# Performance work log

Measured on AMD Instinct MI355X. Metric: run time of the kernel, lower is better.

Reference implementation:

```python
import jax, jax.numpy as jnp
import numpy as np

D_MODEL = 1024
NUM_HEADS = 16
HEAD_DIM = D_MODEL // NUM_HEADS


def setup_inputs() -> dict:
    key = jax.random.key(0)
    ks = jax.random.split(key, 5)
    B, S = 2, 2048
    x = jax.random.normal(ks[0], (B, S, D_MODEL), dtype=jnp.float32)
    # nn.Linear(d,d,bias=False): y = x @ W.T, W is [out,in]. Init ~ U(-1/sqrt(d), 1/sqrt(d)).
    lim = 1.0 / np.sqrt(D_MODEL)
    wq = jax.random.uniform(ks[1], (D_MODEL, D_MODEL), jnp.float32, -lim, lim)
    wk = jax.random.uniform(ks[2], (D_MODEL, D_MODEL), jnp.float32, -lim, lim)
    wv = jax.random.uniform(ks[3], (D_MODEL, D_MODEL), jnp.float32, -lim, lim)
    wo = jax.random.uniform(ks[4], (D_MODEL, D_MODEL), jnp.float32, -lim, lim)
    return {"x": x, "wq": wq, "wk": wk, "wv": wv, "wo": wo}


def reference(x, wq, wk, wv, wo):
    B, S, D = x.shape
    H, Hd = NUM_HEADS, HEAD_DIM
    scale = Hd ** 0.5
    # projections (torch Linear: x @ W.T), split heads -> [B,H,S,Hd]
    q = (x @ wq.T).reshape(B, S, H, Hd).transpose(0, 2, 1, 3)
    k = (x @ wk.T).reshape(B, S, H, Hd).transpose(0, 2, 1, 3)
    v = (x @ wv.T).reshape(B, S, H, Hd).transpose(0, 2, 1, 3)
    scores = jnp.einsum('bhqd,bhkd->bhqk', q, k) / scale  # [B,H,S,S]
    # causal mask: disallow j > i
    causal_mask = jnp.triu(jnp.ones((S, S), dtype=bool), k=1)
    scores = jnp.where(causal_mask, -jnp.inf, scores)
    attn = jax.nn.softmax(scores, axis=-1)
    out = jnp.einsum('bhqk,bhkd->bhqd', attn, v)
    out = out.transpose(0, 2, 1, 3).reshape(B, S, D)
    return out @ wo.T
```

## Files before the change

kernel.cpp:

```cpp
#include <hip/hip_runtime.h>

#define DEV __device__ __forceinline__

typedef __attribute__((ext_vector_type(4))) float f32x4;
typedef __attribute__((ext_vector_type(8))) __bf16 bf16x8;

typedef __attribute__((address_space(1))) const uint32_t gu32;
typedef __attribute__((address_space(3))) uint32_t su32;

DEV void gload16(const void* g, void* s) {
  __builtin_amdgcn_global_load_lds((gu32*)(uintptr_t)g,
                                   (su32*)(uint32_t)(uintptr_t)s, 16, 0, 0);
}

DEV ushort f2bf(float f) {
  unsigned u = __builtin_bit_cast(unsigned, f);
  u = (u + 0x7fffu + ((u >> 16) & 1u)) >> 16;
  return (ushort)u;
}

DEV bf16x8 lds8(const ushort* p) {
  return __builtin_bit_cast(bf16x8, *(const uint4*)(p));
}

__global__ void cvt_bf16(const float* __restrict__ src, ushort* __restrict__ dst, int n4) {
  int i = blockIdx.x * blockDim.x + threadIdx.x;
  if (i >= n4) return;
  float4 v = ((const float4*)src)[i];
  ushort4 o;
  o.x = f2bf(v.x); o.y = f2bf(v.y); o.z = f2bf(v.z); o.w = f2bf(v.w);
  ((ushort4*)dst)[i] = o;
}

template <int F32OUT>
DEV void gemm_core(const ushort* __restrict__ A, const ushort* __restrict__ W,
                   void* __restrict__ Cout, ushort* sA, ushort* sB) {
  const int tid = threadIdx.x;
  const int l = tid & 63, wv = tid >> 6;
  const int g = l >> 4, lan = l & 15;
  const int wr = wv >> 1, wc = wv & 1;
  const int brow = blockIdx.y * 128, bcol = blockIdx.x * 128;

  f32x4 acc[4][4] = {};

  for (int k0 = 0; k0 < 1024; k0 += 32) {
    __syncthreads();
#pragma unroll
    for (int i = 0; i < 2; ++i) {
      int n = i * 256 + wv * 64 + l;
      int row = n >> 2;
      int ss = n & 3;
      int gs = (ss - (row >> 1)) & 3;
      gload16(A + (size_t)(brow + row) * 1024 + k0 + gs * 8,
              sA + (size_t)(i * 256 + wv * 64) * 8);
      gload16(W + (size_t)(bcol + row) * 1024 + k0 + gs * 8,
              sB + (size_t)(i * 256 + wv * 64) * 8);
    }
    __syncthreads();

    bf16x8 a[4], b[4];
#pragma unroll
    for (int fr = 0; fr < 4; ++fr) {
      int row = wr * 64 + fr * 16 + lan;
      a[fr] = lds8(sA + row * 32 + 8 * (((row >> 1) + g) & 3));
    }
#pragma unroll
    for (int fn = 0; fn < 4; ++fn) {
      int row = wc * 64 + fn * 16 + lan;
      b[fn] = lds8(sB + row * 32 + 8 * (((row >> 1) + g) & 3));
    }
#pragma unroll
    for (int fr = 0; fr < 4; ++fr)
#pragma unroll
      for (int fn = 0; fn < 4; ++fn)
        acc[fr][fn] = __builtin_amdgcn_mfma_f32_16x16x32_bf16(a[fr], b[fn], acc[fr][fn], 0, 0, 0);
  }

#pragma unroll
  for (int fr = 0; fr < 4; ++fr)
#pragma unroll
    for (int fn = 0; fn < 4; ++fn)
#pragma unroll
      for (int r = 0; r < 4; ++r) {
        int row = brow + wr * 64 + fr * 16 + g * 4 + r;
        int col = bcol + wc * 64 + fn * 16 + lan;
        if (F32OUT)
          ((float*)Cout)[(size_t)row * 1024 + col] = acc[fr][fn][r];
        else
          ((ushort*)Cout)[(size_t)row * 1024 + col] = f2bf(acc[fr][fn][r]);
      }
}

__global__ __launch_bounds__(256) void gemm_qkv(
    const ushort* __restrict__ X, const ushort* __restrict__ Wq,
    const ushort* __restrict__ Wk, const ushort* __restrict__ Wv,
    ushort* __restrict__ Q, ushort* __restrict__ K, ushort* __restrict__ V) {
  __shared__ __align__(16) ushort sA[4096];
  __shared__ __align__(16) ushort sB[4096];
  const ushort* W = blockIdx.z == 0 ? Wq : (blockIdx.z == 1 ? Wk : Wv);
  ushort* C = blockIdx.z == 0 ? Q : (blockIdx.z == 1 ? K : V);
  gemm_core<0>(X, W, (void*)C, sA, sB);
}

__global__ __launch_bounds__(256) void gemm_out(
    const ushort* __restrict__ AO, const ushort* __restrict__ Wo, float* __restrict__ C) {
  __shared__ __align__(16) ushort sA[4096];
  __shared__ __align__(16) ushort sB[4096];
  gemm_core<1>(AO, Wo, (void*)C, sA, sB);
}

__global__ __launch_bounds__(256) void vt_kernel(const ushort* __restrict__ V,
                                                 ushort* __restrict__ Vt) {
  __shared__ __align__(16) ushort T[64 * 64];
  const int tid = threadIdx.x;
  const int stile = blockIdx.x, bh = blockIdx.y;
  const int b = bh >> 4, h = bh & 15;

#pragma unroll
  for (int i = 0; i < 2; ++i) {
    int m = i * 256 + tid;
    int s = m >> 3, dc = m & 7;
    uint4 v = *(const uint4*)(V + (size_t)(b * 2048 + stile * 64 + s) * 1024 + h * 64 + dc * 8);
    *(uint4*)(T + s * 64 + ((8 * dc) ^ (((s >> 3) & 7) << 3))) = v;
  }
  __syncthreads();

#pragma unroll
  for (int i = 0; i < 2; ++i) {
    int m = i * 256 + tid;
    int d = m >> 3, sb = m & 7;
    ushort tmp[8];
#pragma unroll
    for (int e = 0; e < 8; ++e)
      tmp[e] = T[(sb * 8 + e) * 64 + (d ^ (sb << 3))];
    uint4 o;
    o.x = (uint)tmp[0] | ((uint)tmp[1] << 16);
    o.y = (uint)tmp[2] | ((uint)tmp[3] << 16);
    o.z = (uint)tmp[4] | ((uint)tmp[5] << 16);
    o.w = (uint)tmp[6] | ((uint)tmp[7] << 16);
    *(uint4*)(Vt + ((size_t)bh * 64 + d) * 2048 + stile * 64 + sb * 8) = o;
  }
}

__global__ __launch_bounds__(256) void attn_fwd(
    const ushort* __restrict__ Qm, const ushort* __restrict__ Km,
    const ushort* __restrict__ Vt, ushort* __restrict__ AO) {
  __shared__ __align__(16) ushort sK[64 * 64];
  __shared__ __align__(16) ushort sV[64 * 64];
  __shared__ __align__(16) ushort sP[4 * 16 * 64];

  const int tid = threadIdx.x;
  const int l = tid & 63, wv = tid >> 6;
  const int g = l >> 4, lan = l & 15;
  const int bid = blockIdx.x;
  const int rank = bid >> 5, bh = bid & 31;
  const int qt = 31 - rank;
  const int b = bh >> 4, h = bh & 15;
  const int q0 = qt * 64 + wv * 16;
  const int qg = q0 + lan;

  bf16x8 qf[2];
#pragma unroll
  for (int kf = 0; kf < 2; ++kf)
    qf[kf] = __builtin_bit_cast(bf16x8,
        *(const uint4*)(Qm + (size_t)(b * 2048 + qg) * 1024 + h * 64 + kf * 32 + g * 8));

  float mrun = -1e30f, lrun = 0.f;
  f32x4 o[4];
#pragma unroll
  for (int of = 0; of < 4; ++of) o[of] = (f32x4){0.f, 0.f, 0.f, 0.f};

  ushort* Pw = sP + wv * 1024;
  const int nkt = qt + 1;

  for (int kt = 0; kt < nkt; ++kt) {
    __syncthreads();
#pragma unroll
    for (int i = 0; i < 2; ++i) {
      int n = i * 256 + wv * 64 + l;
      int row = n >> 3, ss = n & 7, gs = ss ^ (row & 7);
      gload16(Km + (size_t)(b * 2048 + kt * 64 + row) * 1024 + h * 64 + gs * 8,
              sK + (size_t)(i * 256 + wv * 64) * 8);
      gload16(Vt + ((size_t)bh * 64 + row) * 2048 + kt * 64 + gs * 8,
              sV + (size_t)(i * 256 + wv * 64) * 8);
    }
    __syncthreads();

    f32x4 sc[4];
    __builtin_amdgcn_s_setprio(1);
#pragma unroll
    for (int kvf = 0; kvf < 4; ++kvf) {
      f32x4 acc = (f32x4){0.f, 0.f, 0.f, 0.f};
#pragma unroll
      for (int kf = 0; kf < 2; ++kf) {
        int row = kvf * 16 + lan;
        bf16x8 kb = lds8(sK + row * 64 + 8 * ((kf * 4 + g) ^ (row & 7)));
        acc = __builtin_amdgcn_mfma_f32_16x16x32_bf16(kb, qf[kf], acc, 0, 0, 0);
      }
      sc[kvf] = acc;
    }
    __builtin_amdgcn_s_setprio(0);

    float mx = -1e30f;
#pragma unroll
    for (int kvf = 0; kvf < 4; ++kvf)
#pragma unroll
      for (int r = 0; r < 4; ++r) {
        int kvg = kt * 64 + kvf * 16 + 4 * g + r;
        float v = sc[kvf][r] * 0.125f;
        v = (kvg <= qg) ? v : -1e30f;
        sc[kvf][r] = v;
        mx = fmaxf(mx, v);
      }
    mx = fmaxf(mx, __shfl_xor(mx, 16));
    mx = fmaxf(mx, __shfl_xor(mx, 32));
    float mnew = fmaxf(mrun, mx);
    float alpha = __expf(mrun - mnew);
    mrun = mnew;
    float rs = 0.f;
#pragma unroll
    for (int kvf = 0; kvf < 4; ++kvf)
#pragma unroll
      for (int r = 0; r < 4; ++r) {
        float p = __expf(sc[kvf][r] - mnew);
        sc[kvf][r] = p;
        rs += p;
      }
    rs += __shfl_xor(rs, 16);
    rs += __shfl_xor(rs, 32);
    lrun = lrun * alpha + rs;

#pragma unroll
    for (int kvf = 0; kvf < 4; ++kvf) {
      ushort4 pk;
      pk.x = f2bf(sc[kvf][0]); pk.y = f2bf(sc[kvf][1]);
      pk.z = f2bf(sc[kvf][2]); pk.w = f2bf(sc[kvf][3]);
      *(ushort4*)(Pw + lan * 64 + ((16 * kvf + 4 * g) ^ ((lan & 7) << 3))) = pk;
    }

    float al[4];
#pragma unroll
    for (int r = 0; r < 4; ++r) al[r] = __shfl(alpha, g * 4 + r);
#pragma unroll
    for (int of = 0; of < 4; ++of)
#pragma unroll
      for (int r = 0; r < 4; ++r) o[of][r] *= al[r];

    bf16x8 pa[2];
#pragma unroll
    for (int kf = 0; kf < 2; ++kf)
      pa[kf] = lds8(Pw + lan * 64 + ((32 * kf + 8 * g) ^ ((lan & 7) << 3)));

    __builtin_amdgcn_s_setprio(1);
#pragma unroll
    for (int of = 0; of < 4; ++of) {
#pragma unroll
      for (int kf = 0; kf < 2; ++kf) {
        int row = of * 16 + lan;
        bf16x8 vb = lds8(sV + row * 64 + 8 * ((kf * 4 + g) ^ (row & 7)));
        o[of] = __builtin_amdgcn_mfma_f32_16x16x32_bf16(pa[kf], vb, o[of], 0, 0, 0);
      }
    }
    __builtin_amdgcn_s_setprio(0);
  }

#pragma unroll
  for (int r = 0; r < 4; ++r) {
    float il = 1.0f / __shfl(lrun, g * 4 + r);
#pragma unroll
    for (int of = 0; of < 4; ++of) {
      int grow = qt * 64 + wv * 16 + g * 4 + r;
      AO[(size_t)(b * 2048 + grow) * 1024 + h * 64 + of * 16 + lan] = f2bf(o[of][r] * il);
    }
  }
}

extern "C" void kernel_launch(void* const* d_in, const int* in_sizes, int n_in,
                              void* d_out, int out_size, void* d_ws, size_t ws_size,
                              hipStream_t stream) {
  const float* x  = (const float*)d_in[0];
  const float* wq = (const float*)d_in[1];
  const float* wk = (const float*)d_in[2];
  const float* wv = (const float*)d_in[3];
  const float* wo = (const float*)d_in[4];
  float* out = (float*)d_out;

  char* ws = (char*)d_ws;
  const size_t MB = 1ull << 20;
  ushort* xb  = (ushort*)(ws + 0);
  ushort* wqb = (ushort*)(ws + 8 * MB);
  ushort* wkb = (ushort*)(ws + 10 * MB);
  ushort* wvb = (ushort*)(ws + 12 * MB);
  ushort* wob = (ushort*)(ws + 14 * MB);
  ushort* Q   = (ushort*)(ws + 16 * MB);
  ushort* K   = (ushort*)(ws + 24 * MB);
  ushort* V   = (ushort*)(ws + 32 * MB);
  ushort* AO  = (ushort*)(ws + 40 * MB);
  ushort* Vt  = (ushort*)(ws + 0);

  cvt_bf16<<<4096, 256, 0, stream>>>(x, xb, 1048576);
  cvt_bf16<<<1024, 256, 0, stream>>>(wq, wqb, 262144);
  cvt_bf16<<<1024, 256, 0, stream>>>(wk, wkb, 262144);
  cvt_bf16<<<1024, 256, 0, stream>>>(wv, wvb, 262144);
  cvt_bf16<<<1024, 256, 0, stream>>>(wo, wob, 262144);

  gemm_qkv<<<dim3(8, 32, 3), 256, 0, stream>>>(xb, wqb, wkb, wvb, Q, K, V);
  vt_kernel<<<dim3(32, 32), 256, 0, stream>>>(V, Vt);
  attn_fwd<<<1024, 256, 0, stream>>>(Q, K, Vt, AO);
  gemm_out<<<dim3(8, 32), 256, 0, stream>>>(AO, wob, out);
}
```

Baseline: 198.3 us.

## Double-buffer GEMM and attention loads, fuse conversions, fold softmax scale into Wq

Merges the five fp32-to-bf16 conversion launches into one kernel, and pre-scales Wq by log2(e)/8 so attention can use exp2 without a per-element scale. Both GEMMs and the attention loop now double-buffer their LDS tiles, so the next tile's global loads overlap the current MFMA work, with a single vmcnt wait and barrier per step. The output GEMM uses narrower 128x64 tiles to launch more blocks. Attention applies the causal mask only on the diagonal tile and skips rescaling the accumulator while the running max grows by at most 8. That skip risks a small loss of accuracy, and the extra LDS buffers can lower occupancy.

```diff
diff --git a/kernel.cpp b/kernel.cpp
--- a/kernel.cpp
+++ b/kernel.cpp
@@ -13,100 +13,132 @@
                                    (su32*)(uint32_t)(uintptr_t)s, 16, 0, 0);
 }
 
-DEV ushort f2bf(float f) {
-  unsigned u = __builtin_bit_cast(unsigned, f);
-  u = (u + 0x7fffu + ((u >> 16) & 1u)) >> 16;
-  return (ushort)u;
-}
+DEV ushort bfbits(float f) { return __builtin_bit_cast(ushort, (__bf16)f); }
 
 DEV bf16x8 lds8(const ushort* p) {
   return __builtin_bit_cast(bf16x8, *(const uint4*)(p));
 }
 
-__global__ void cvt_bf16(const float* __restrict__ src, ushort* __restrict__ dst, int n4) {
+DEV void vmcnt0bar() {
+  asm volatile("s_waitcnt vmcnt(0)" ::: "memory");
+  __builtin_amdgcn_s_barrier();
+}
+
+__global__ void cvt_all(const float* __restrict__ x, const float* __restrict__ wq,
+                        const float* __restrict__ wk, const float* __restrict__ wv,
+                        const float* __restrict__ wo, ushort* __restrict__ xb,
+                        ushort* __restrict__ wb) {
   int i = blockIdx.x * blockDim.x + threadIdx.x;
-  if (i >= n4) return;
-  float4 v = ((const float4*)src)[i];
+  const float* src; ushort* dst; float scl = 1.0f; int j;
+  if (i < 1048576) { src = x; dst = xb; j = i; }
+  else {
+    int t = (i - 1048576) >> 18;
+    j = (i - 1048576) & 262143;
+    src = t == 0 ? wq : (t == 1 ? wk : (t == 2 ? wv : wo));
+    dst = wb + t * 1048576;
+    if (t == 0) scl = 0.18033688011f;
+  }
+  float4 v = ((const float4*)src)[j];
   ushort4 o;
-  o.x = f2bf(v.x); o.y = f2bf(v.y); o.z = f2bf(v.z); o.w = f2bf(v.w);
-  ((ushort4*)dst)[i] = o;
-}
-
-template <int F32OUT>
+  o.x = bfbits(v.x * scl); o.y = bfbits(v.y * scl);
+  o.z = bfbits(v.z * scl); o.w = bfbits(v.w * scl);
+  ((ushort4*)dst)[j] = o;
+}
+
+template <int NFR, int F32OUT>
 DEV void gemm_core(const ushort* __restrict__ A, const ushort* __restrict__ W,
                    void* __restrict__ Cout, ushort* sA, ushort* sB) {
   const int tid = threadIdx.x;
   const int l = tid & 63, wv = tid >> 6;
   const int g = l >> 4, lan = l & 15;
   const int wr = wv >> 1, wc = wv & 1;
-  const int brow = blockIdx.y * 128, bcol = blockIdx.x * 128;
-
-  f32x4 acc[4][4] = {};
-
-  for (int k0 = 0; k0 < 1024; k0 += 32) {
-    __syncthreads();
+  const int brow = blockIdx.y * 128, bcol = blockIdx.x * (NFR * 32);
+  const int ASZ = 128 * 32, BSZ = NFR * 32 * 32;
+
+  f32x4 acc[4][NFR] = {};
+
+  auto stage = [&](int buf, int k0) {
+    ushort* dA = sA + buf * ASZ;
+    ushort* dB = sB + buf * BSZ;
 #pragma unroll
     for (int i = 0; i < 2; ++i) {
       int n = i * 256 + wv * 64 + l;
-      int row = n >> 2;
-      int ss = n & 3;
-      int gs = (ss - (row >> 1)) & 3;
+      int row = n >> 2, ss = n & 3, gs = (ss - (row >> 1)) & 3;
       gload16(A + (size_t)(brow + row) * 1024 + k0 + gs * 8,
-              sA + (size_t)(i * 256 + wv * 64) * 8);
+              dA + (i * 256 + wv * 64) * 8);
+    }
+#pragma unroll
+    for (int i = 0; i < NFR / 2; ++i) {
+      int n = i * 256 + wv * 64 + l;
+      int row = n >> 2, ss = n & 3, gs = (ss - (row >> 1)) & 3;
       gload16(W + (size_t)(bcol + row) * 1024 + k0 + gs * 8,
-              sB + (size_t)(i * 256 + wv * 64) * 8);
-    }
-    __syncthreads();
-
-    bf16x8 a[4], b[4];
+              dB + (i * 256 + wv * 64) * 8);
+    }
+  };
+
+  auto compute = [&](int buf) {
+    const ushort* cA = sA + buf * ASZ;
+    const ushort* cB = sB + buf * BSZ;
+    bf16x8 a[4], b[NFR];
 #pragma unroll
     for (int fr = 0; fr < 4; ++fr) {
       int row = wr * 64 + fr * 16 + lan;
-      a[fr] = lds8(sA + row * 32 + 8 * (((row >> 1) + g) & 3));
-    }
-#pragma unroll
-    for (int fn = 0; fn < 4; ++fn) {
-      int row = wc * 64 + fn * 16 + lan;
-      b[fn] = lds8(sB + row * 32 + 8 * (((row >> 1) + g) & 3));
-    }
+      a[fr] = lds8(cA + row * 32 + 8 * (((row >> 1) + g) & 3));
+    }
+#pragma unroll
+    for (int fn = 0; fn < NFR; ++fn) {
+      int row = wc * (NFR * 16) + fn * 16 + lan;
+      b[fn] = lds8(cB + row * 32 + 8 * (((row >> 1) + g) & 3));
+    }
+    __builtin_amdgcn_s_setprio(1);
 #pragma unroll
     for (int fr = 0; fr < 4; ++fr)
 #pragma unroll
-      for (int fn = 0; fn < 4; ++fn)
+      for (int fn = 0; fn < NFR; ++fn)
         acc[fr][fn] = __builtin_amdgcn_mfma_f32_16x16x32_bf16(a[fr], b[fn], acc[fr][fn], 0, 0, 0);
-  }
+    __builtin_amdgcn_s_setprio(0);
+  };
+
+  stage(0, 0);
+  vmcnt0bar();
+#pragma unroll 1
+  for (int t = 0; t < 15; ++t) {
+    stage(1, (2 * t + 1) * 32); compute(0); vmcnt0bar();
+    stage(0, (2 * t + 2) * 32); compute(1); vmcnt0bar();
+  }
+  stage(1, 31 * 32); compute(0); vmcnt0bar();
+  compute(1);
 
 #pragma unroll
   for (int fr = 0; fr < 4; ++fr)
 #pragma unroll
-    for (int fn = 0; fn < 4; ++fn)
+    for (int fn = 0; fn < NFR; ++fn)
 #pragma unroll
       for (int r = 0; r < 4; ++r) {
         int row = brow + wr * 64 + fr * 16 + g * 4 + r;
-        int col = bcol + wc * 64 + fn * 16 + lan;
+        int col = bcol + wc * (NFR * 16) + fn * 16 + lan;
         if (F32OUT)
           ((float*)Cout)[(size_t)row * 1024 + col] = acc[fr][fn][r];
         else
-          ((ushort*)Cout)[(size_t)row * 1024 + col] = f2bf(acc[fr][fn][r]);
+          ((ushort*)Cout)[(size_t)row * 1024 + col] = bfbits(acc[fr][fn][r]);
       }
 }
 
 __global__ __launch_bounds__(256) void gemm_qkv(
-    const ushort* __restrict__ X, const ushort* __restrict__ Wq,
-    const ushort* __restrict__ Wk, const ushort* __restrict__ Wv,
+    const ushort* __restrict__ X, const ushort* __restrict__ Wb,
     ushort* __restrict__ Q, ushort* __restrict__ K, ushort* __restrict__ V) {
-  __shared__ __align__(16) ushort sA[4096];
-  __shared__ __align__(16) ushort sB[4096];
-  const ushort* W = blockIdx.z == 0 ? Wq : (blockIdx.z == 1 ? Wk : Wv);
+  __shared__ __align__(16) ushort sA[2 * 128 * 32];
+  __shared__ __align__(16) ushort sB[2 * 128 * 32];
+  const ushort* W = Wb + (size_t)blockIdx.z * 1048576;
   ushort* C = blockIdx.z == 0 ? Q : (blockIdx.z == 1 ? K : V);
-  gemm_core<0>(X, W, (void*)C, sA, sB);
+  gemm_core<4, 0>(X, W, (void*)C, sA, sB);
 }
 
 __global__ __launch_bounds__(256) void gemm_out(
     const ushort* __restrict__ AO, const ushort* __restrict__ Wo, float* __restrict__ C) {
-  __shared__ __align__(16) ushort sA[4096];
-  __shared__ __align__(16) ushort sB[4096];
-  gemm_core<1>(AO, Wo, (void*)C, sA, sB);
+  __shared__ __align__(16) ushort sA[2 * 128 * 32];
+  __shared__ __align__(16) ushort sB[2 * 64 * 32];
+  gemm_core<2, 1>(AO, Wo, (void*)C, sA, sB);
 }
 
 __global__ __launch_bounds__(256) void vt_kernel(const ushort* __restrict__ V,
@@ -145,8 +177,8 @@
 __global__ __launch_bounds__(256) void attn_fwd(
     const ushort* __restrict__ Qm, const ushort* __restrict__ Km,
     const ushort* __restrict__ Vt, ushort* __restrict__ AO) {
-  __shared__ __align__(16) ushort sK[64 * 64];
-  __shared__ __align__(16) ushort sV[64 * 64];
+  __shared__ __align__(16) ushort sK[2][64 * 64];
+  __shared__ __align__(16) ushort sV[2][64 * 64];
   __shared__ __align__(16) ushort sP[4 * 16 * 64];
 
   const int tid = threadIdx.x;
@@ -173,79 +205,96 @@
   ushort* Pw = sP + wv * 1024;
   const int nkt = qt + 1;
 
-  for (int kt = 0; kt < nkt; ++kt) {
-    __syncthreads();
+  auto stagekv = [&](int buf, int kt) {
 #pragma unroll
     for (int i = 0; i < 2; ++i) {
       int n = i * 256 + wv * 64 + l;
       int row = n >> 3, ss = n & 7, gs = ss ^ (row & 7);
       gload16(Km + (size_t)(b * 2048 + kt * 64 + row) * 1024 + h * 64 + gs * 8,
-              sK + (size_t)(i * 256 + wv * 64) * 8);
+              sK[buf] + (i * 256 + wv * 64) * 8);
       gload16(Vt + ((size_t)bh * 64 + row) * 2048 + kt * 64 + gs * 8,
-              sV + (size_t)(i * 256 + wv * 64) * 8);
-    }
-    __syncthreads();
+              sV[buf] + (i * 256 + wv * 64) * 8);
+    }
+  };
+
+  stagekv(0, 0);
+  vmcnt0bar();
+
+#pragma unroll 1
+  for (int kt = 0; kt < nkt; ++kt) {
+    const int buf = kt & 1;
+    if (kt + 1 < nkt) stagekv(buf ^ 1, kt + 1);
 
     f32x4 sc[4];
     __builtin_amdgcn_s_setprio(1);
 #pragma unroll
     for (int kvf = 0; kvf < 4; ++kvf) {
-      f32x4 acc = (f32x4){0.f, 0.f, 0.f, 0.f};
+      f32x4 a2 = (f32x4){0.f, 0.f, 0.f, 0.f};
 #pragma unroll
       for (int kf = 0; kf < 2; ++kf) {
         int row = kvf * 16 + lan;
-        bf16x8 kb = lds8(sK + row * 64 + 8 * ((kf * 4 + g) ^ (row & 7)));
-        acc = __builtin_amdgcn_mfma_f32_16x16x32_bf16(kb, qf[kf], acc, 0, 0, 0);
+        bf16x8 kb = lds8(sK[buf] + row * 64 + 8 * ((kf * 4 + g) ^ (row & 7)));
+        a2 = __builtin_amdgcn_mfma_f32_16x16x32_bf16(kb, qf[kf], a2, 0, 0, 0);
       }
-      sc[kvf] = acc;
+      sc[kvf] = a2;
     }
     __builtin_amdgcn_s_setprio(0);
 
-    float mx = -1e30f;
+    if (kt == qt) {
+#pragma unroll
+      for (int kvf = 0; kvf < 4; ++kvf)
+#pragma unroll
+        for (int r = 0; r < 4; ++r) {
+          int kvg = kt * 64 + kvf * 16 + 4 * g + r;
+          sc[kvf][r] = (kvg <= qg) ? sc[kvf][r] : -1e30f;
+        }
+    }
+
+    float mx = sc[0][0];
 #pragma unroll
     for (int kvf = 0; kvf < 4; ++kvf)
 #pragma unroll
-      for (int r = 0; r < 4; ++r) {
-        int kvg = kt * 64 + kvf * 16 + 4 * g + r;
-        float v = sc[kvf][r] * 0.125f;
-        v = (kvg <= qg) ? v : -1e30f;
-        sc[kvf][r] = v;
-        mx = fmaxf(mx, v);
-      }
+      for (int r = 0; r < 4; ++r) mx = fmaxf(mx, sc[kvf][r]);
     mx = fmaxf(mx, __shfl_xor(mx, 16));
     mx = fmaxf(mx, __shfl_xor(mx, 32));
-    float mnew = fmaxf(mrun, mx);
-    float alpha = __expf(mrun - mnew);
-    mrun = mnew;
+
+    const bool noresc = __all(mx <= mrun + 8.0f);
+    const float mnew = noresc ? mrun : fmaxf(mrun, mx);
+
     float rs = 0.f;
 #pragma unroll
     for (int kvf = 0; kvf < 4; ++kvf)
 #pragma unroll
       for (int r = 0; r < 4; ++r) {
-        float p = __expf(sc[kvf][r] - mnew);
+        float p = __builtin_exp2f(sc[kvf][r] - mnew);
         sc[kvf][r] = p;
         rs += p;
       }
     rs += __shfl_xor(rs, 16);
     rs += __shfl_xor(rs, 32);
-    lrun = lrun * alpha + rs;
+
+    if (noresc) {
+      lrun += rs;
+    } else {
+      float alpha = __builtin_exp2f(mrun - mnew);
+      mrun = mnew;
+      lrun = lrun * alpha + rs;
+      float al[4];
+#pragma unroll
+      for (int r = 0; r < 4; ++r) al[r] = __shfl(alpha, g * 4 + r);
+#pragma unroll
+      for (int of = 0; of < 4; ++of)
+#pragma unroll
+        for (int r = 0; r < 4; ++r) o[of][r] *= al[r];
+    }
 
 #pragma unroll
     for (int kvf = 0; kvf < 4; ++kvf) {
       ushort4 pk;
-      pk.x = f2bf(sc[kvf][0]); pk.y = f2bf(sc[kvf][1]);
-      pk.z = f2bf(sc[kvf][2]); pk.w = f2bf(sc[kvf][3]);
+      pk.x = bfbits(sc[kvf][0]); pk.y = bfbits(sc[kvf][1]);
+      pk.z = bfbits(sc[kvf][2]); pk.w = bfbits(sc[kvf][3]);
       *(ushort4*)(Pw + lan * 64 + ((16 * kvf + 4 * g) ^ ((lan & 7) << 3))) = pk;
     }
-
-    float al[4];
-#pragma unroll
-    for (int r = 0; r < 4; ++r) al[r] = __shfl(alpha, g * 4 + r);
-#pragma unroll
-    for (int of = 0; of < 4; ++of)
-#pragma unroll
-      for (int r = 0; r < 4; ++r) o[of][r] *= al[r];
-
     bf16x8 pa[2];
 #pragma unroll
     for (int kf = 0; kf < 2; ++kf)
@@ -253,15 +302,16 @@
 
     __builtin_amdgcn_s_setprio(1);
 #pragma unroll
-    for (int of = 0; of < 4; ++of) {
+    for (int of = 0; of < 4; ++of)
 #pragma unroll
       for (int kf = 0; kf < 2; ++kf) {
         int row = of * 16 + lan;
-        bf16x8 vb = lds8(sV + row * 64 + 8 * ((kf * 4 + g) ^ (row & 7)));
+        bf16x8 vb = lds8(sV[buf] + row * 64 + 8 * ((kf * 4 + g) ^ (row & 7)));
         o[of] = __builtin_amdgcn_mfma_f32_16x16x32_bf16(pa[kf], vb, o[of], 0, 0, 0);
       }
-    }
     __builtin_amdgcn_s_setprio(0);
+
+    vmcnt0bar();
   }
 
 #pragma unroll
@@ -270,7 +320,7 @@
 #pragma unroll
     for (int of = 0; of < 4; ++of) {
       int grow = qt * 64 + wv * 16 + g * 4 + r;
-      AO[(size_t)(b * 2048 + grow) * 1024 + h * 64 + of * 16 + lan] = f2bf(o[of][r] * il);
+      AO[(size_t)(b * 2048 + grow) * 1024 + h * 64 + of * 16 + lan] = bfbits(o[of][r] * il);
     }
   }
 }
@@ -287,25 +337,18 @@
 
   char* ws = (char*)d_ws;
   const size_t MB = 1ull << 20;
-  ushort* xb  = (ushort*)(ws + 0);
-  ushort* wqb = (ushort*)(ws + 8 * MB);
-  ushort* wkb = (ushort*)(ws + 10 * MB);
-  ushort* wvb = (ushort*)(ws + 12 * MB);
-  ushort* wob = (ushort*)(ws + 14 * MB);
-  ushort* Q   = (ushort*)(ws + 16 * MB);
-  ushort* K   = (ushort*)(ws + 24 * MB);
-  ushort* V   = (ushort*)(ws + 32 * MB);
-  ushort* AO  = (ushort*)(ws + 40 * MB);
-  ushort* Vt  = (ushort*)(ws + 0);
-
-  cvt_bf16<<<4096, 256, 0, stream>>>(x, xb, 1048576);
-  cvt_bf16<<<1024, 256, 0, stream>>>(wq, wqb, 262144);
-  cvt_bf16<<<1024, 256, 0, stream>>>(wk, wkb, 262144);
-  cvt_bf16<<<1024, 256, 0, stream>>>(wv, wvb, 262144);
-  cvt_bf16<<<1024, 256, 0, stream>>>(wo, wob, 262144);
-
-  gemm_qkv<<<dim3(8, 32, 3), 256, 0, stream>>>(xb, wqb, wkb, wvb, Q, K, V);
+  ushort* xb = (ushort*)(ws + 0);
+  ushort* wb = (ushort*)(ws + 8 * MB);
+  ushort* Q  = (ushort*)(ws + 16 * MB);
+  ushort* K  = (ushort*)(ws + 24 * MB);
+  ushort* V  = (ushort*)(ws + 32 * MB);
+  ushort* AO = (ushort*)(ws + 40 * MB);
+  ushort* Vt = (ushort*)(ws + 0);
+  ushort* wob = wb + 3 * 1048576;
+
+  cvt_all<<<8192, 256, 0, stream>>>(x, wq, wk, wv, wo, xb, wb);
+  gemm_qkv<<<dim3(8, 32, 3), 256, 0, stream>>>(xb, wb, Q, K, V);
   vt_kernel<<<dim3(32, 32), 256, 0, stream>>>(V, Vt);
   attn_fwd<<<1024, 256, 0, stream>>>(Q, K, Vt, AO);
-  gemm_out<<<dim3(8, 32), 256, 0, stream>>>(AO, wob, out);
-}
+  gemm_out<<<dim3(16, 32), 256, 0, stream>>>(AO, wob, out);
+}
```

Result: faster. 184.4 us (-7.0%).
